# Kernel optimization log

Measured on AMD Instinct MI355X. Metric: run time of the kernel, lower is better.

## Reference

```python
import jax, jax.numpy as jnp
import numpy as np

B, S, H = 4, 1024, 1024
NH = 16
D = H // NH  # attention_head_size = 64
L = 9        # num_labels
MAXREL = 5
B_PERSON = 1
I_PERSON = 2
LN_EPS = 1e-5


def setup_inputs() -> dict:
    key = jax.random.key(0)
    ks = jax.random.split(key, 16)
    lin = lambda k, i, o: 0.02 * jax.random.normal(k, (i, o), jnp.float32)
    return {
        "sequence_output": jax.random.normal(ks[0], (B, S, H), jnp.float32),
        "Wq": lin(ks[1], H, H), "bq": jnp.zeros((H,), jnp.float32),
        "Wk": lin(ks[2], H, H), "bk": jnp.zeros((H,), jnp.float32),
        "Wv": lin(ks[3], H, H), "bv": jnp.zeros((H,), jnp.float32),
        "Wo": lin(ks[4], H, H), "bo": jnp.zeros((H,), jnp.float32),
        "ln_g": jnp.ones((H,), jnp.float32), "ln_b": jnp.zeros((H,), jnp.float32),
        "Ws": lin(ks[5], H, L), "bs": jnp.zeros((L,), jnp.float32),
        "entity_bias": 0.1 * jax.random.normal(ks[6], (L,), jnp.float32),
        "rel_pos_emb": jax.random.normal(ks[7], (2 * MAXREL + 1, D), jnp.float32),  # declared but unused in forward math, matching the torch module
    }


def reference(sequence_output, Wq, bq, Wk, bk, Wv, bv, Wo, bo, ln_g, ln_b, Ws, bs, entity_bias, rel_pos_emb):
    x = sequence_output  # [B,S,H]
    b, s, _ = x.shape

    def heads(t):  # [B,S,H] -> [B,NH,S,D]
        return t.reshape(b, s, NH, D).transpose(0, 2, 1, 3)

    q = heads(x @ Wq + bq)
    k = heads(x @ Wk + bk)
    v = heads(x @ Wv + bv)

    scores = jnp.einsum('bhqd,bhkd->bhqk', q, k)  # [B,NH,S,S]

    r = jnp.arange(s, dtype=jnp.float32)
    dist = jnp.abs(r[:, None] - r[None, :])                 # |i-j|, [S,S]
    pos_bias = jnp.exp(-0.1 * jnp.clip(dist, 0.0, float(MAXREL)))
    # torch order: (scores + pos_bias) / sqrt(D) + distance_mask
    scores = (scores + pos_bias) / np.sqrt(D) + (-0.1) * dist

    probs = jax.nn.softmax(scores, axis=-1)  # dropout is identity in eval
    ctx = jnp.einsum('bhqk,bhkd->bhqd', probs, v)
    ctx = ctx.transpose(0, 2, 1, 3).reshape(b, s, H)

    y = x + (ctx @ Wo + bo)  # residual
    mu = y.mean(-1, keepdims=True)
    var = y.var(-1, keepdims=True)
    yn = (y - mu) / jnp.sqrt(var + LN_EPS) * ln_g + ln_b

    span_logits = yn @ Ws + bs  # [B,S,L]
    # entity-bias loop: if argmax(span_logits[i,j-1]) == B-PERSON, add entity_bias[I-PERSON] twice to final[i,j,I-PERSON]
    prev_is_b = (jnp.argmax(span_logits[:, :-1, :], axis=-1) == B_PERSON).astype(span_logits.dtype)  # [B,S-1]
    final_logits = span_logits.at[:, 1:, I_PERSON].add(2.0 * entity_bias[I_PERSON] * prev_is_b)
    return final_logits
```

## Files before the change

### kernel.cpp

```cpp
#include <hip/hip_runtime.h>
#include <hip/hip_bf16.h>
#include <math.h>

typedef unsigned short ush;
typedef __attribute__((ext_vector_type(8))) _Float16 fragh;
typedef __attribute__((ext_vector_type(4))) _Float16 half4;
typedef __attribute__((ext_vector_type(4))) float f32x4;

#define S_   1024
#define H_   1024
#define NH_  16
#define D_   64
#define L_   9
#define MB_  (1048576ull)

__device__ __forceinline__ void load_lds16(const ush* g, const ush* l) {
  __builtin_amdgcn_global_load_lds(
      (const __attribute__((address_space(1))) void*)g,
      (__attribute__((address_space(3))) void*)l, 16, 0, 0);
}

__global__ __launch_bounds__(256) void cast_wT4(
    const float* W0, const float* W1, const float* W2, const float* W3,
    ush* T0, ush* T1, ush* T2, ush* T3) {
  __shared__ __align__(16) float Ls[64][68];
  const float* W = (blockIdx.z == 0) ? W0 : (blockIdx.z == 1) ? W1
                 : (blockIdx.z == 2) ? W2 : W3;
  ush* Th = (blockIdx.z == 0) ? T0 : (blockIdx.z == 1) ? T1
          : (blockIdx.z == 2) ? T2 : T3;
  const int tid = threadIdx.x;
  const int n0 = blockIdx.x * 64, k0 = blockIdx.y * 64;
#pragma unroll
  for (int it = 0; it < 4; it++) {
    int flat = tid + 256 * it;
    int row = flat >> 4, nc = (flat & 15) * 4;
    *(float4*)&Ls[row][nc] = *(const float4*)&W[(size_t)(k0 + row) * 1024 + n0 + nc];
  }
  __syncthreads();
#pragma unroll
  for (int it = 0; it < 2; it++) {
    int flat = tid + 256 * it;
    int nrow = flat >> 3, kc = (flat & 7) * 8;
    fragh v;
#pragma unroll
    for (int u = 0; u < 8; u++) v[u] = (_Float16)Ls[kc + u][nrow];
    *(fragh*)&Th[(size_t)(n0 + nrow) * 1024 + k0 + kc] = v;
  }
}

__global__ __launch_bounds__(256) void cast_x(
    const float* __restrict__ x, ush* __restrict__ xh) {
  const size_t i = ((size_t)blockIdx.x * 256 + threadIdx.x) * 8;
  float4 a = *(const float4*)&x[i];
  float4 b = *(const float4*)&x[i + 4];
  fragh v;
  v[0] = (_Float16)a.x; v[1] = (_Float16)a.y;
  v[2] = (_Float16)a.z; v[3] = (_Float16)a.w;
  v[4] = (_Float16)b.x; v[5] = (_Float16)b.y;
  v[6] = (_Float16)b.z; v[7] = (_Float16)b.w;
  *(fragh*)&xh[i] = v;
}

__global__ __launch_bounds__(256) void gemm_qkv(
    const ush* __restrict__ xh,
    const ush* __restrict__ Bq, const ush* __restrict__ Bk,
    const ush* __restrict__ Bv,
    const float* __restrict__ bq, const float* __restrict__ bk,
    const float* __restrict__ bv,
    ush* __restrict__ qh, ush* __restrict__ kh, ush* __restrict__ vT) {
  __shared__ __align__(16) ush As[2][128][32];
  __shared__ __align__(16) ush Bs[2][128][32];
  const int tid = threadIdx.x, lane = tid & 63, wave = tid >> 6;
  const int l15 = lane & 15, quad = lane >> 4;
  const int m0 = blockIdx.y * 128, n0 = blockIdx.x * 128;
  const int z = blockIdx.z;
  const ush* Bg = (z == 0) ? Bq : (z == 1) ? Bk : Bv;
  const float* bias = (z == 0) ? bq : (z == 1) ? bk : bv;
  ush* outp = (z == 0) ? qh : (z == 1) ? kh : vT;

  const int wm = (wave >> 1) * 64, wn = (wave & 1) * 64;

  f32x4 acc[4][4];
#pragma unroll
  for (int i = 0; i < 4; i++)
#pragma unroll
    for (int j = 0; j < 4; j++) acc[i][j] = (f32x4){0.f, 0.f, 0.f, 0.f};

  auto stage = [&](int bi, int k0) {
#pragma unroll
    for (int jj = 0; jj < 2; jj++) {
      const int call = wave * 2 + jj;
      const int c = call * 64 + lane;
      const int r = c >> 2, ch = c & 3;
      load_lds16(xh + (size_t)(m0 + r) * 1024 + k0 + ch * 8,
                 &As[bi][0][0] + (size_t)call * 512);
    }
#pragma unroll
    for (int jj = 0; jj < 2; jj++) {
      const int call = wave * 2 + jj;
      const int c = call * 64 + lane;
      const int r = c >> 2, ch = c & 3;
      load_lds16(Bg + (size_t)(n0 + r) * 1024 + k0 + ch * 8,
                 &Bs[bi][0][0] + (size_t)call * 512);
    }
  };

  stage(0, 0);
  __syncthreads();

  for (int k0 = 0; k0 < 1024; k0 += 32) {
    const int cur = (k0 >> 5) & 1;
    if (k0 + 32 < 1024) stage(cur ^ 1, k0 + 32);

    fragh a[4], b[4];
#pragma unroll
    for (int s = 0; s < 4; s++)
      a[s] = *(const fragh*)&As[cur][wm + s * 16 + l15][quad * 8];
#pragma unroll
    for (int t = 0; t < 4; t++)
      b[t] = *(const fragh*)&Bs[cur][wn + t * 16 + l15][quad * 8];
#pragma unroll
    for (int mi = 0; mi < 4; mi++)
#pragma unroll
      for (int ni = 0; ni < 4; ni++)
        acc[mi][ni] = __builtin_amdgcn_mfma_f32_16x16x32_f16(
            a[mi], b[ni], acc[mi][ni], 0, 0, 0);
    __syncthreads();
  }

#pragma unroll
  for (int mi = 0; mi < 4; mi++) {
    const int rbase = m0 + wm + mi * 16 + quad * 4;
    const int bb = rbase >> 10, ss = rbase & 1023;
#pragma unroll
    for (int ni = 0; ni < 4; ni++) {
      const int col = n0 + wn + ni * 16 + l15;
      const float bv_ = bias[col];
      const int hidx = col >> 6, d = col & 63;
      if (z == 2) {
        half4 p4;
        p4[0] = (_Float16)(acc[mi][ni][0] + bv_);
        p4[1] = (_Float16)(acc[mi][ni][1] + bv_);
        p4[2] = (_Float16)(acc[mi][ni][2] + bv_);
        p4[3] = (_Float16)(acc[mi][ni][3] + bv_);
        *(half4*)&outp[((size_t)(bb * NH_ + hidx) * D_ + d) * S_ + ss] = p4;
      } else {
#pragma unroll
        for (int r = 0; r < 4; r++) {
          const size_t o =
              ((size_t)(bb * NH_ + hidx) * S_ + (ss + r)) * D_ + d;
          *(_Float16*)&outp[o] = (_Float16)(acc[mi][ni][r] + bv_);
        }
      }
    }
  }
}

__global__ __launch_bounds__(256) void gemm_o(
    const ush* __restrict__ ctxh, const ush* __restrict__ Bo,
    const float* __restrict__ bo, const float* __restrict__ resid,
    float* __restrict__ outf) {
  __shared__ __align__(16) ush As[2][128][32];
  __shared__ __align__(16) ush Bs[2][64][32];
  const int tid = threadIdx.x, lane = tid & 63, wave = tid >> 6;
  const int l15 = lane & 15, quad = lane >> 4;
  const int m0 = blockIdx.y * 128, n0 = blockIdx.x * 64;
  const int wm = (wave >> 1) * 64, wn = (wave & 1) * 32;

  f32x4 acc[4][2];
#pragma unroll
  for (int i = 0; i < 4; i++)
#pragma unroll
    for (int j = 0; j < 2; j++) acc[i][j] = (f32x4){0.f, 0.f, 0.f, 0.f};

  auto stage = [&](int bi, int k0) {
#pragma unroll
    for (int jj = 0; jj < 2; jj++) {
      const int call = wave * 2 + jj;
      const int c = call * 64 + lane;
      const int r = c >> 2, ch = c & 3;
      load_lds16(ctxh + (size_t)(m0 + r) * 1024 + k0 + ch * 8,
                 &As[bi][0][0] + (size_t)call * 512);
    }
    {
      const int c = wave * 64 + lane;
      const int r = c >> 2, ch = c & 3;
      load_lds16(Bo + (size_t)(n0 + r) * 1024 + k0 + ch * 8,
                 &Bs[bi][0][0] + (size_t)wave * 512);
    }
  };

  stage(0, 0);
  __syncthreads();

  for (int k0 = 0; k0 < 1024; k0 += 32) {
    const int cur = (k0 >> 5) & 1;
    if (k0 + 32 < 1024) stage(cur ^ 1, k0 + 32);

    fragh a[4], b[2];
#pragma unroll
    for (int s = 0; s < 4; s++)
      a[s] = *(const fragh*)&As[cur][wm + s * 16 + l15][quad * 8];
#pragma unroll
    for (int t = 0; t < 2; t++)
      b[t] = *(const fragh*)&Bs[cur][wn + t * 16 + l15][quad * 8];
#pragma unroll
    for (int mi = 0; mi < 4; mi++)
#pragma unroll
      for (int ni = 0; ni < 2; ni++)
        acc[mi][ni] = __builtin_amdgcn_mfma_f32_16x16x32_f16(
            a[mi], b[ni], acc[mi][ni], 0, 0, 0);
    __syncthreads();
  }

#pragma unroll
  for (int mi = 0; mi < 4; mi++) {
    const int rbase = m0 + wm + mi * 16 + quad * 4;
#pragma unroll
    for (int ni = 0; ni < 2; ni++) {
      const int col = n0 + wn + ni * 16 + l15;
      const float bv_ = bo[col];
#pragma unroll
      for (int r = 0; r < 4; r++) {
        const int m = rbase + r;
        outf[(size_t)m * 1024 + col] =
            acc[mi][ni][r] + bv_ + resid[(size_t)m * 1024 + col];
      }
    }
  }
}

__global__ __launch_bounds__(256) void attn2(
    const ush* __restrict__ qh, const ush* __restrict__ kh,
    const ush* __restrict__ vT, ush* __restrict__ ch) {
  __shared__ __align__(16) ush Kh[64][72];
  __shared__ __align__(16) ush VTs[64][72];
  __shared__ __align__(16) ush Pst[64][72];
  __shared__ float LUT[256];
  const int tid = threadIdx.x;
  const int lane = tid & 63, wave = tid >> 6;
  const int l15 = lane & 15, quad = lane >> 4;
  const int w16 = wave * 16;
  const int bh = blockIdx.y;
  const int b = bh >> 4, h = bh & 15;
  const int q0 = blockIdx.x * 64;

  const float K1 = 0.18033688011112042f;
  const float K2 = 0.14426950408889634f;
  {
    const float dd = (float)tid;
    LUT[tid] = __expf(-0.1f * fminf(dd, 5.0f)) * K1 - dd * K2
             - 2.8853900817779268f;
  }

  const size_t qrow = ((size_t)bh * S_ + q0 + w16 + l15) * D_;
  fragh a_h[2];
  a_h[0] = *(const fragh*)&qh[qrow + quad * 8];
  a_h[1] = *(const fragh*)&qh[qrow + 32 + quad * 8];

  f32x4 o[4];
  float lrow[4];
#pragma unroll
  for (int i = 0; i < 4; i++) {
    o[i] = (f32x4){0.f, 0.f, 0.f, 0.f};
    lrow[i] = 0.f;
  }

  const size_t kbase = (size_t)bh * S_ * D_;
  const size_t vbase = (size_t)bh * D_ * S_;

  const int jlo = (q0 > 128) ? q0 - 128 : 0;
  const int jend = (q0 + 192 < S_) ? q0 + 192 : S_;

  for (int j0 = jlo; j0 < jend; j0 += 64) {
    __syncthreads();
#pragma unroll
    for (int it = 0; it < 2; it++) {
      const int flat = tid + 256 * it;
      const int row = flat >> 3, dc = (flat & 7) * 8;
      *(uint4*)&Kh[row][dc] =
          *(const uint4*)&kh[kbase + (size_t)(j0 + row) * D_ + dc];
      *(uint4*)&VTs[row][dc] =
          *(const uint4*)&vT[vbase + (size_t)row * S_ + j0 + dc];
    }
    __syncthreads();

    f32x4 c4[4];
#pragma unroll
    for (int nt = 0; nt < 4; nt++) c4[nt] = (f32x4){0.f, 0.f, 0.f, 0.f};
#pragma unroll
    for (int kk = 0; kk < 2; kk++) {
#pragma unroll
      for (int nt = 0; nt < 4; nt++) {
        fragh bh_ = *(const fragh*)&Kh[nt * 16 + l15][kk * 32 + quad * 8];
        c4[nt] = __builtin_amdgcn_mfma_f32_16x16x32_f16(a_h[kk], bh_, c4[nt], 0, 0, 0);
      }
    }

    const int ib = q0 + w16 + quad * 4 - j0 - l15;
#pragma unroll
    for (int r = 0; r < 4; r++) {
#pragma unroll
      for (int nt = 0; nt < 4; nt++) {
        int di = ib + r - nt * 16;
        di = (di < 0) ? -di : di;
        const float sv = exp2f(fmaf(c4[nt][r], K1, LUT[di]));
        lrow[r] += sv;
        *(_Float16*)&Pst[w16 + quad * 4 + r][nt * 16 + l15] = (_Float16)sv;
      }
    }

    fragh pa[2];
    pa[0] = *(const fragh*)&Pst[w16 + l15][quad * 8];
    pa[1] = *(const fragh*)&Pst[w16 + l15][32 + quad * 8];
#pragma unroll
    for (int dt = 0; dt < 4; dt++) {
      fragh vb0 = *(const fragh*)&VTs[dt * 16 + l15][quad * 8];
      fragh vb1 = *(const fragh*)&VTs[dt * 16 + l15][32 + quad * 8];
      o[dt] = __builtin_amdgcn_mfma_f32_16x16x32_f16(pa[0], vb0, o[dt], 0, 0, 0);
      o[dt] = __builtin_amdgcn_mfma_f32_16x16x32_f16(pa[1], vb1, o[dt], 0, 0, 0);
    }
  }

#pragma unroll
  for (int r = 0; r < 4; r++) {
#pragma unroll
    for (int off = 1; off < 16; off <<= 1) lrow[r] += __shfl_xor(lrow[r], off);
    const float inv = 1.0f / lrow[r];
    const size_t rowp =
        ((size_t)(b * S_ + q0 + w16 + quad * 4 + r)) * H_ + h * 64;
#pragma unroll
    for (int dt = 0; dt < 4; dt++)
      *(_Float16*)&ch[rowp + dt * 16 + l15] = (_Float16)(o[dt][r] * inv);
  }
}

__global__ __launch_bounds__(256) void ln_span(
    const float* __restrict__ y, const float* __restrict__ g,
    const float* __restrict__ bta, const float* __restrict__ Wsp,
    const float* __restrict__ bs, float* __restrict__ logits) {
  const int row = blockIdx.x;
  const int tid = threadIdx.x, lane = tid & 63, wave = tid >> 6;
  const float* yr = y + (size_t)row * 1024;
  float vals[4], s = 0.f, s2 = 0.f;
#pragma unroll
  for (int i = 0; i < 4; i++) {
    float t = yr[tid + i * 256];
    vals[i] = t; s += t; s2 += t * t;
  }
#pragma unroll
  for (int off = 32; off; off >>= 1) {
    s += __shfl_xor(s, off);
    s2 += __shfl_xor(s2, off);
  }
  __shared__ float red[8];
  __shared__ float red9[4][12];
  if (lane == 0) { red[wave] = s; red[4 + wave] = s2; }
  __syncthreads();
  s = red[0] + red[1] + red[2] + red[3];
  s2 = red[4] + red[5] + red[6] + red[7];
  const float mu = s * (1.0f / 1024.0f);
  const float var = s2 * (1.0f / 1024.0f) - mu * mu;
  const float inv = rsqrtf(var + 1e-5f);

  float lg[9];
#pragma unroll
  for (int l = 0; l < 9; l++) lg[l] = 0.f;
#pragma unroll
  for (int i = 0; i < 4; i++) {
    const int hh = tid + i * 256;
    const float yn = (vals[i] - mu) * inv * g[hh] + bta[hh];
#pragma unroll
    for (int l = 0; l < 9; l++) lg[l] += yn * Wsp[hh * 9 + l];
  }
#pragma unroll
  for (int l = 0; l < 9; l++) {
#pragma unroll
    for (int off = 32; off; off >>= 1) lg[l] += __shfl_xor(lg[l], off);
  }
  if (lane == 0) {
#pragma unroll
    for (int l = 0; l < 9; l++) red9[wave][l] = lg[l];
  }
  __syncthreads();
  if (tid < 9) {
    logits[(size_t)row * 9 + tid] =
        red9[0][tid] + red9[1][tid] + red9[2][tid] + red9[3][tid] + bs[tid];
  }
}

__global__ __launch_bounds__(256) void final_kernel(
    const float* __restrict__ logits, const float* __restrict__ eb,
    float* __restrict__ out) {
  const int m = blockIdx.x * 256 + threadIdx.x;
  const int i = m & 1023;
  float cur[9];
#pragma unroll
  for (int l = 0; l < 9; l++) cur[l] = logits[(size_t)m * 9 + l];
  if (i > 0) {
    const float* prev = logits + (size_t)(m - 1) * 9;
    int am = 0;
    float best = prev[0];
#pragma unroll
    for (int l = 1; l < 9; l++) {
      float pv = prev[l];
      if (pv > best) { best = pv; am = l; }
    }
    if (am == 1) cur[2] += 2.0f * eb[2];
  }
#pragma unroll
  for (int l = 0; l < 9; l++) out[(size_t)m * 9 + l] = cur[l];
}

extern "C" void kernel_launch(void* const* d_in, const int* in_sizes, int n_in,
                              void* d_out, int out_size, void* d_ws, size_t ws_size,
                              hipStream_t stream) {
  const float* x    = (const float*)d_in[0];
  const float* Wq   = (const float*)d_in[1];
  const float* bq   = (const float*)d_in[2];
  const float* Wk   = (const float*)d_in[3];
  const float* bk   = (const float*)d_in[4];
  const float* Wv   = (const float*)d_in[5];
  const float* bv   = (const float*)d_in[6];
  const float* Wo   = (const float*)d_in[7];
  const float* bo   = (const float*)d_in[8];
  const float* ln_g = (const float*)d_in[9];
  const float* ln_b = (const float*)d_in[10];
  const float* Ws   = (const float*)d_in[11];
  const float* bs   = (const float*)d_in[12];
  const float* eb   = (const float*)d_in[13];
  float* out = (float*)d_out;
  char* W8 = (char*)d_ws;

  ush* WoT  = (ush*)(W8 + 0 * MB_);
  ush* WqT  = (ush*)(W8 + 2 * MB_);
  ush* WkT  = (ush*)(W8 + 4 * MB_);
  ush* WvT  = (ush*)(W8 + 6 * MB_);
  ush* xh   = (ush*)(W8 + 8 * MB_);
  ush* qh   = (ush*)(W8 + 16 * MB_);
  ush* kh   = (ush*)(W8 + 24 * MB_);
  ush* vT   = (ush*)(W8 + 32 * MB_);
  ush* ctxh = (ush*)(W8 + 40 * MB_);
  float* y_ws  = (float*)(W8 + 48 * MB_);
  float* lg_ws = (float*)(W8 + 16 * MB_);

  cast_wT4<<<dim3(16, 16, 4), 256, 0, stream>>>(
      Wq, Wk, Wv, Wo, WqT, WkT, WvT, WoT);
  cast_x<<<2048, 256, 0, stream>>>(x, xh);

  gemm_qkv<<<dim3(8, 32, 3), 256, 0, stream>>>(
      xh, WqT, WkT, WvT, bq, bk, bv, qh, kh, vT);
  attn2<<<dim3(16, 64), 256, 0, stream>>>(qh, kh, vT, ctxh);
  gemm_o<<<dim3(16, 32), 256, 0, stream>>>(ctxh, WoT, bo, x, y_ws);
  ln_span<<<4096, 256, 0, stream>>>(y_ws, ln_g, ln_b, Ws, bs, lg_ws);
  final_kernel<<<16, 256, 0, stream>>>(lg_ws, eb, out);
}
```

Before: 203.3 us.

## Use partial vmcnt waits to overlap next-tile LDS loads with MFMA in GEMMs

Restructures the double-buffered K loops of the QKV projection and output projection GEMMs. Instead of __syncthreads, which drains all outstanding global-to-LDS loads, each iteration issues the next stage, waits only for the previous stage's loads with a partial s_waitcnt vmcnt, and then issues raw s_barriers, so next-tile loads stay in flight during the MFMAs. The QKV compute also loads B fragments one at a time, interleaved with MFMAs, to lower register pressure. The hand-set vmcnt counts must match the number of loads issued per stage, otherwise LDS reads race with loads still in flight.

```diff
diff --git a/kernel.cpp b/kernel.cpp
--- a/kernel.cpp
+++ b/kernel.cpp
@@ -105,28 +105,39 @@
     }
   };
 
-  stage(0, 0);
-  __syncthreads();
-
-  for (int k0 = 0; k0 < 1024; k0 += 32) {
-    const int cur = (k0 >> 5) & 1;
-    if (k0 + 32 < 1024) stage(cur ^ 1, k0 + 32);
-
-    fragh a[4], b[4];
+  auto compute = [&](int cur) {
+    fragh a[4], b[2][2];
 #pragma unroll
     for (int s = 0; s < 4; s++)
       a[s] = *(const fragh*)&As[cur][wm + s * 16 + l15][quad * 8];
 #pragma unroll
-    for (int t = 0; t < 4; t++)
-      b[t] = *(const fragh*)&Bs[cur][wn + t * 16 + l15][quad * 8];
-#pragma unroll
-    for (int mi = 0; mi < 4; mi++)
-#pragma unroll
-      for (int ni = 0; ni < 4; ni++)
-        acc[mi][ni] = __builtin_amdgcn_mfma_f32_16x16x32_f16(
-            a[mi], b[ni], acc[mi][ni], 0, 0, 0);
-    __syncthreads();
-  }
+    for (int t = 0; t < 4; t++) {
+      fragh bt = *(const fragh*)&Bs[cur][wn + t * 16 + l15][quad * 8];
+#pragma unroll
+      for (int mi = 0; mi < 4; mi++)
+        acc[mi][t] = __builtin_amdgcn_mfma_f32_16x16x32_f16(
+            a[mi], bt, acc[mi][t], 0, 0, 0);
+    }
+    (void)b;
+  };
+
+  stage(0, 0);
+#pragma unroll 1
+  for (int t = 0; t < 31; ++t) {
+    const int cur = t & 1;
+    stage(cur ^ 1, (t + 1) << 5);
+    __builtin_amdgcn_sched_barrier(0);
+    asm volatile("s_waitcnt vmcnt(4)" ::: "memory");
+    __builtin_amdgcn_sched_barrier(0);
+    __builtin_amdgcn_s_barrier();
+    compute(cur);
+    __builtin_amdgcn_s_barrier();
+  }
+  __builtin_amdgcn_sched_barrier(0);
+  asm volatile("s_waitcnt vmcnt(0)" ::: "memory");
+  __builtin_amdgcn_sched_barrier(0);
+  __builtin_amdgcn_s_barrier();
+  compute(1);
 
 #pragma unroll
   for (int mi = 0; mi < 4; mi++) {
@@ -190,13 +201,7 @@
     }
   };
 
-  stage(0, 0);
-  __syncthreads();
-
-  for (int k0 = 0; k0 < 1024; k0 += 32) {
-    const int cur = (k0 >> 5) & 1;
-    if (k0 + 32 < 1024) stage(cur ^ 1, k0 + 32);
-
+  auto compute = [&](int cur) {
     fragh a[4], b[2];
 #pragma unroll
     for (int s = 0; s < 4; s++)
@@ -210,8 +215,25 @@
       for (int ni = 0; ni < 2; ni++)
         acc[mi][ni] = __builtin_amdgcn_mfma_f32_16x16x32_f16(
             a[mi], b[ni], acc[mi][ni], 0, 0, 0);
-    __syncthreads();
-  }
+  };
+
+  stage(0, 0);
+#pragma unroll 1
+  for (int t = 0; t < 31; ++t) {
+    const int cur = t & 1;
+    stage(cur ^ 1, (t + 1) << 5);
+    __builtin_amdgcn_sched_barrier(0);
+    asm volatile("s_waitcnt vmcnt(3)" ::: "memory");
+    __builtin_amdgcn_sched_barrier(0);
+    __builtin_amdgcn_s_barrier();
+    compute(cur);
+    __builtin_amdgcn_s_barrier();
+  }
+  __builtin_amdgcn_sched_barrier(0);
+  asm volatile("s_waitcnt vmcnt(0)" ::: "memory");
+  __builtin_amdgcn_sched_barrier(0);
+  __builtin_amdgcn_s_barrier();
+  compute(1);
 
 #pragma unroll
   for (int mi = 0; mi < 4; mi++) {
```

New measurement: 203.0 us. About the same (-0.2%).
